# Kernel tuning notes

Hardware: AMD Instinct MI355X
Metric: run time of the kernel (lower is better)

Reference implementation:

```python
import jax, jax.numpy as jnp
import numpy as np

NUM_BASES = 8


def setup_inputs() -> dict:
    key = jax.random.key(0)
    ks = jax.random.split(key, 8)
    N, E = 100000, 1600000
    IN_F, OUT_F, NUM_RELS = 128, 128, 16
    si = IN_F // NUM_BASES   # 16
    so = OUT_F // NUM_BASES  # 16
    return {
        "h": jax.random.normal(ks[0], (N, IN_F), dtype=jnp.float32),
        "norm": jax.random.uniform(ks[1], (N, 1), dtype=jnp.float32),
        "edge_src": jax.random.randint(ks[2], (E,), 0, N, dtype=jnp.int32),
        "edge_dst": jax.random.randint(ks[3], (E,), 0, N, dtype=jnp.int32),
        "edge_type": jax.random.randint(ks[4], (E,), 0, NUM_RELS, dtype=jnp.int32),
        "weight": jax.random.normal(ks[5], (NUM_RELS, NUM_BASES * si * so), dtype=jnp.float32) * 0.1,
        "bias_param": jax.random.normal(ks[6], (OUT_F,), dtype=jnp.float32) * 0.1,
        "loop_weight": jax.random.normal(ks[7], (IN_F, OUT_F), dtype=jnp.float32) * 0.1,
    }


def reference(h, norm, edge_src, edge_dst, edge_type, weight, bias_param, loop_weight):
    N, in_feat = h.shape
    out_feat = loop_weight.shape[1]
    si = in_feat // NUM_BASES
    so = out_feat // NUM_BASES
    E = edge_type.shape[0]

    # self-loop message (dropout=0.0 -> identity)
    loop_message = h @ loop_weight                      # [N, out_feat]

    # msg_func: gather per-edge relation weight blocks and do block-diag bmm
    W = weight[edge_type].reshape(E, NUM_BASES, si, so)  # [E, B, si, so]
    src = h[edge_src].reshape(E, NUM_BASES, si)          # [E, B, si]
    msg = jnp.einsum("ebi,ebio->ebo", src, W).reshape(E, out_feat)

    # scatter-sum messages to destination nodes, rescale by norm
    agg = jax.ops.segment_sum(msg, edge_dst, num_segments=N)  # [N, out_feat]
    node_repr = agg * norm

    # bias + self-loop + activation
    node_repr = node_repr + bias_param + loop_message
    return jax.nn.relu(node_repr)
```

## Files before the change

kernel.cpp:

```cpp
#include <hip/hip_runtime.h>


__device__ __forceinline__ unsigned int f2bf(float f) {
  const unsigned int u = __float_as_uint(f);
  return (u + 0x7FFFu + ((u >> 16) & 1u)) >> 16;
}

__global__ __launch_bounds__(256) void rgcn_init_kernel(
    const float* __restrict__ h, const float* __restrict__ loop_w,
    const float* __restrict__ bias, float* __restrict__ out, int N) {
  __shared__ float lw[128 * 128];
  for (int idx = threadIdx.x; idx < 128 * 128 / 4; idx += 256) {
    ((float4*)lw)[idx] = ((const float4*)loop_w)[idx];
  }
  __syncthreads();

  const int lane = threadIdx.x & 63;
  const int wid = threadIdx.x >> 6;
  const int group0 = blockIdx.x * 4 + wid;
  const int ngroups = gridDim.x * 4;
  const int totgroups = (N + 3) >> 2;
  const float b0 = bias[lane];
  const float b1 = bias[64 + lane];

  for (int g = group0; g < totgroups; g += ngroups) {
    const int n0 = g * 4;
    const int nn = (N - n0 < 4) ? (N - n0) : 4;
    if (nn == 4) {
      const float* __restrict__ r0 = h + (size_t)n0 * 128;
      const float* __restrict__ r1 = r0 + 128;
      const float* __restrict__ r2 = r1 + 128;
      const float* __restrict__ r3 = r2 + 128;
      float a00 = b0, a01 = b1, a10 = b0, a11 = b1;
      float a20 = b0, a21 = b1, a30 = b0, a31 = b1;
#pragma unroll 4
      for (int k = 0; k < 128; ++k) {
        const float w0 = lw[k * 128 + lane];
        const float w1 = lw[k * 128 + 64 + lane];
        a00 = fmaf(r0[k], w0, a00); a01 = fmaf(r0[k], w1, a01);
        a10 = fmaf(r1[k], w0, a10); a11 = fmaf(r1[k], w1, a11);
        a20 = fmaf(r2[k], w0, a20); a21 = fmaf(r2[k], w1, a21);
        a30 = fmaf(r3[k], w0, a30); a31 = fmaf(r3[k], w1, a31);
      }
      float* __restrict__ o0 = out + (size_t)n0 * 128;
      o0[lane] = a00;        o0[64 + lane] = a01;
      o0[128 + lane] = a10;  o0[192 + lane] = a11;
      o0[256 + lane] = a20;  o0[320 + lane] = a21;
      o0[384 + lane] = a30;  o0[448 + lane] = a31;
    } else {
      for (int r = 0; r < nn; ++r) {
        const int n = n0 + r;
        const float* __restrict__ hr = h + (size_t)n * 128;
        float a0 = b0, a1 = b1;
#pragma unroll 4
        for (int k = 0; k < 128; ++k) {
          const float a = hr[k];
          a0 = fmaf(a, lw[k * 128 + lane], a0);
          a1 = fmaf(a, lw[k * 128 + 64 + lane], a1);
        }
        out[(size_t)n * 128 + lane] = a0;
        out[(size_t)n * 128 + 64 + lane] = a1;
      }
    }
  }
}

__global__ __launch_bounds__(1024) void rgcn_precompute_kernel(
    const float* __restrict__ h, const float* __restrict__ weight,
    unsigned int* __restrict__ M, int base, int cend) {
  const int lane = threadIdx.x & 63;
  const int t = threadIdx.x >> 6;
  const int b = lane >> 4;
  const int o = lane & 15;

  const float* __restrict__ wb = weight + t * 2048 + b * 256 + o;
  float wlo[16], whi[16];
#pragma unroll
  for (int i = 0; i < 16; ++i) {
    wlo[i] = wb[i * 16];
    whi[i] = wb[1024 + i * 16];
  }

  const int span = cend - base;
  const int n0 = base + (int)(((long)blockIdx.x * span) / gridDim.x);
  const int n1 = base + (int)(((long)(blockIdx.x + 1) * span) / gridDim.x);

#pragma unroll 2
  for (int n = n0; n < n1; ++n) {
    const float4* __restrict__ hp =
        (const float4*)(h + (size_t)n * 128) + (b << 2);
    const float4 x0 = hp[0], x1 = hp[1], x2 = hp[2], x3 = hp[3];
    const float4 y0 = hp[16], y1 = hp[17], y2 = hp[18], y3 = hp[19];

    float a0 = x0.x * wlo[0], a1 = x0.y * wlo[1];
    a0 = fmaf(x0.z, wlo[2], a0);  a1 = fmaf(x0.w, wlo[3], a1);
    a0 = fmaf(x1.x, wlo[4], a0);  a1 = fmaf(x1.y, wlo[5], a1);
    a0 = fmaf(x1.z, wlo[6], a0);  a1 = fmaf(x1.w, wlo[7], a1);
    a0 = fmaf(x2.x, wlo[8], a0);  a1 = fmaf(x2.y, wlo[9], a1);
    a0 = fmaf(x2.z, wlo[10], a0); a1 = fmaf(x2.w, wlo[11], a1);
    a0 = fmaf(x3.x, wlo[12], a0); a1 = fmaf(x3.y, wlo[13], a1);
    a0 = fmaf(x3.z, wlo[14], a0); a1 = fmaf(x3.w, wlo[15], a1);

    float c0 = y0.x * whi[0], c1 = y0.y * whi[1];
    c0 = fmaf(y0.z, whi[2], c0);  c1 = fmaf(y0.w, whi[3], c1);
    c0 = fmaf(y1.x, whi[4], c0);  c1 = fmaf(y1.y, whi[5], c1);
    c0 = fmaf(y1.z, whi[6], c0);  c1 = fmaf(y1.w, whi[7], c1);
    c0 = fmaf(y2.x, whi[8], c0);  c1 = fmaf(y2.y, whi[9], c1);
    c0 = fmaf(y2.z, whi[10], c0); c1 = fmaf(y2.w, whi[11], c1);
    c0 = fmaf(y3.x, whi[12], c0); c1 = fmaf(y3.y, whi[13], c1);
    c0 = fmaf(y3.z, whi[14], c0); c1 = fmaf(y3.w, whi[15], c1);

    const unsigned int pk = f2bf(a0 + a1) | (f2bf(c0 + c1) << 16);
    M[(((size_t)(n - base) << 4) | t) * 64 + lane] = pk;
  }
}

__global__ __launch_bounds__(256) void rgcn_zero_kernel(int* __restrict__ p,
                                                        int n) {
  for (int i = blockIdx.x * 256 + threadIdx.x; i < n; i += gridDim.x * 256)
    p[i] = 0;
}

__global__ __launch_bounds__(256) void rgcn_hist_kernel(
    const int* __restrict__ esrc, const int* __restrict__ edst,
    int* __restrict__ cnt, int E, int N, unsigned S) {
  for (int e = blockIdx.x * 256 + threadIdx.x; e < E; e += gridDim.x * 256) {
    const unsigned q = (unsigned)esrc[e] / S;
    atomicAdd(&cnt[(int)(q * (unsigned)N) + edst[e]], 1);
  }
}

__global__ __launch_bounds__(1024) void rgcn_scan_pass1(
    const int* __restrict__ cnt, int* __restrict__ partial, int bins) {
  __shared__ int sums[1024];
  const int t = threadIdx.x;
  const int base = blockIdx.x * 4096 + t * 4;
  int s = 0;
  if (base + 3 < bins) {
    const int4 v = *(const int4*)(cnt + base);
    s = v.x + v.y + v.z + v.w;
  } else {
    for (int j = 0; j < 4; ++j)
      if (base + j < bins) s += cnt[base + j];
  }
  sums[t] = s;
  __syncthreads();
  for (int off = 512; off > 0; off >>= 1) {
    if (t < off) sums[t] += sums[t + off];
    __syncthreads();
  }
  if (t == 0) partial[blockIdx.x] = sums[0];
}

__global__ __launch_bounds__(1024) void rgcn_scan_pass2(
    int* __restrict__ partial, int nb) {
  __shared__ int sc[1024];
  const int t = threadIdx.x;
  int v[4];
  int s = 0;
#pragma unroll
  for (int j = 0; j < 4; ++j) {
    const int i = t * 4 + j;
    v[j] = (i < nb) ? partial[i] : 0;
    s += v[j];
  }
  sc[t] = s;
  __syncthreads();
#pragma unroll
  for (int off = 1; off < 1024; off <<= 1) {
    const int add = (t >= off) ? sc[t - off] : 0;
    __syncthreads();
    sc[t] += add;
    __syncthreads();
  }
  int run = (t == 0) ? 0 : sc[t - 1];
#pragma unroll
  for (int j = 0; j < 4; ++j) {
    const int i = t * 4 + j;
    if (i < nb) partial[i] = run;
    run += v[j];
  }
}

__global__ __launch_bounds__(1024) void rgcn_scan_pass3(
    const int* __restrict__ cnt, const int* __restrict__ partial,
    int* __restrict__ row_ptr, int* __restrict__ cursor, int bins) {
  __shared__ int sums[1024];
  const int t = threadIdx.x;
  const int base = blockIdx.x * 4096 + t * 4;
  int v0 = 0, v1 = 0, v2 = 0, v3 = 0;
  if (base + 3 < bins) {
    const int4 v = *(const int4*)(cnt + base);
    v0 = v.x; v1 = v.y; v2 = v.z; v3 = v.w;
  } else {
    if (base < bins) v0 = cnt[base];
    if (base + 1 < bins) v1 = cnt[base + 1];
    if (base + 2 < bins) v2 = cnt[base + 2];
  }
  sums[t] = v0 + v1 + v2 + v3;
  __syncthreads();
#pragma unroll
  for (int off = 1; off < 1024; off <<= 1) {
    const int add = (t >= off) ? sums[t - off] : 0;
    __syncthreads();
    sums[t] += add;
    __syncthreads();
  }
  const int run = partial[blockIdx.x] + ((t == 0) ? 0 : sums[t - 1]);
  const int p0 = run, p1 = p0 + v0, p2 = p1 + v1, p3 = p2 + v2;
  if (base + 3 < bins) {
    *(int4*)(row_ptr + base) = make_int4(p0, p1, p2, p3);
    *(int4*)(cursor + base) = make_int4(p0, p1, p2, p3);
  } else {
    if (base < bins) { row_ptr[base] = p0; cursor[base] = p0; }
    if (base + 1 < bins) { row_ptr[base + 1] = p1; cursor[base + 1] = p1; }
    if (base + 2 < bins) { row_ptr[base + 2] = p2; cursor[base + 2] = p2; }
  }
}

__global__ void rgcn_set_kernel(int* __restrict__ p, int v) {
  if (threadIdx.x == 0) *p = v;
}

__global__ __launch_bounds__(256) void rgcn_scatter_kernel(
    const int* __restrict__ esrc, const int* __restrict__ edst,
    const int* __restrict__ etype, int* __restrict__ cursor,
    int* __restrict__ srec, int E, int N, unsigned S) {
  for (int e = blockIdx.x * 256 + threadIdx.x; e < E; e += gridDim.x * 256) {
    const unsigned s = (unsigned)esrc[e];
    const unsigned q = s / S;
    const int key = (int)(q * (unsigned)N) + edst[e];
    const int p = atomicAdd(&cursor[key], 1);
    srec[p] = (int)((s - q * S) << 4) | etype[e];
  }
}

__global__ __launch_bounds__(256) void rgcn_gather3_kernel(
    const float* __restrict__ norm, const int* __restrict__ srec,
    const int* __restrict__ rpc, const unsigned int* __restrict__ M,
    float* __restrict__ out, int N, int final_pass) {
  const int lane = threadIdx.x & 63;
  const int w0 = blockIdx.x * 4 + (threadIdx.x >> 6);
  const int nw = gridDim.x * 4;

  for (int d = w0; d < N; d += nw) {
    const int e0 = rpc[d];
    const int e1 = rpc[d + 1];
    if (!final_pass && e0 == e1) continue;

    float acc0 = 0.f, acc1 = 0.f;
    int e = e0;
    for (; e + 4 <= e1; e += 4) {
      const int r0 = srec[e], r1 = srec[e + 1], r2 = srec[e + 2],
                r3 = srec[e + 3];
      const unsigned int v0 = M[(size_t)r0 * 64 + lane];
      const unsigned int v1 = M[(size_t)r1 * 64 + lane];
      const unsigned int v2 = M[(size_t)r2 * 64 + lane];
      const unsigned int v3 = M[(size_t)r3 * 64 + lane];
      acc0 += __uint_as_float(v0 << 16);
      acc1 += __uint_as_float(v0 & 0xFFFF0000u);
      acc0 += __uint_as_float(v1 << 16);
      acc1 += __uint_as_float(v1 & 0xFFFF0000u);
      acc0 += __uint_as_float(v2 << 16);
      acc1 += __uint_as_float(v2 & 0xFFFF0000u);
      acc0 += __uint_as_float(v3 << 16);
      acc1 += __uint_as_float(v3 & 0xFFFF0000u);
    }
    for (; e < e1; ++e) {
      const unsigned int v = M[(size_t)srec[e] * 64 + lane];
      acc0 += __uint_as_float(v << 16);
      acc1 += __uint_as_float(v & 0xFFFF0000u);
    }

    const float nm = norm[d];
    float* __restrict__ op = out + ((size_t)d << 7);
    float o0 = fmaf(acc0, nm, op[lane]);
    float o1 = fmaf(acc1, nm, op[64 + lane]);
    if (final_pass) {
      o0 = fmaxf(o0, 0.f);
      o1 = fmaxf(o1, 0.f);
    }
    op[lane] = o0;
    op[64 + lane] = o1;
  }
}

__global__ __launch_bounds__(256) void rgcn_edge_kernel(
    const float* __restrict__ h, const float* __restrict__ norm,
    const int* __restrict__ esrc, const int* __restrict__ edst,
    const int* __restrict__ etype, const float* __restrict__ weight,
    float* __restrict__ out, int E) {
  const int lane = threadIdx.x & 63;
  const int wid = threadIdx.x >> 6;
  const int wave0 = blockIdx.x * 4 + wid;
  const int nwaves = gridDim.x * 4;
  const int b = lane >> 4;
  const int o = lane & 15;

  for (int e = wave0; e < E; e += nwaves) {
    const int src = esrc[e];
    const int dst = edst[e];
    const int et = etype[e];
    const float s_lo = h[src * 128 + lane];
    const float s_hi = h[src * 128 + 64 + lane];
    const float nrm = norm[dst];
    const float* __restrict__ Wb = weight + et * 2048 + b * 256 + o;
    float m0 = 0.f, m1 = 0.f;
#pragma unroll
    for (int i = 0; i < 16; ++i) {
      const float a_lo = __shfl(s_lo, (lane & 48) + i, 64);
      const float a_hi = __shfl(s_hi, (lane & 48) + i, 64);
      m0 = fmaf(a_lo, Wb[i * 16], m0);
      m1 = fmaf(a_hi, Wb[1024 + i * 16], m1);
    }
    atomicAdd(&out[dst * 128 + lane], m0 * nrm);
    atomicAdd(&out[dst * 128 + 64 + lane], m1 * nrm);
  }
}

__global__ __launch_bounds__(256) void rgcn_relu_kernel(float* __restrict__ out,
                                                        int total4) {
  int i = blockIdx.x * 256 + threadIdx.x;
  const int stride = gridDim.x * 256;
  for (; i < total4; i += stride) {
    float4 v = ((float4*)out)[i];
    v.x = fmaxf(v.x, 0.f);
    v.y = fmaxf(v.y, 0.f);
    v.z = fmaxf(v.z, 0.f);
    v.w = fmaxf(v.w, 0.f);
    ((float4*)out)[i] = v;
  }
}

extern "C" void kernel_launch(void* const* d_in, const int* in_sizes, int n_in,
                              void* d_out, int out_size, void* d_ws, size_t ws_size,
                              hipStream_t stream) {
  const float* h      = (const float*)d_in[0];
  const float* norm   = (const float*)d_in[1];
  const int*   esrc   = (const int*)d_in[2];
  const int*   edst   = (const int*)d_in[3];
  const int*   etype  = (const int*)d_in[4];
  const float* weight = (const float*)d_in[5];
  const float* bias   = (const float*)d_in[6];
  const float* loop_w = (const float*)d_in[7];
  float* out = (float*)d_out;

  const int N = in_sizes[0] / 128;
  const int E = in_sizes[2];
  const int nrels = in_sizes[5] / 2048;

  rgcn_init_kernel<<<2048, 256, 0, stream>>>(h, loop_w, bias, out, N);

  int C = -1, S = 0;
  size_t ofs_rp = 0, ofs_cur = 0, ofs_part = 0, ofs_srec = 0, ofs_M = 0;
  if (nrels == 16 && N >= 1 && N < (1 << 26)) {
    for (int cc = 1; cc <= 64; ++cc) {
      const size_t bins = (size_t)cc * (size_t)N;
      if (bins > (size_t)4096 * 4096) break;
      const int ss = (N + cc - 1) / cc;
      const size_t o_rp = (bins + 3) & ~(size_t)3;
      const size_t o_cur = (o_rp + bins + 1 + 3) & ~(size_t)3;
      const size_t o_part = (o_cur + bins + 3) & ~(size_t)3;
      const size_t o_srec = o_part + 4096;
      const size_t o_M = (o_srec + (size_t)E + 15) & ~(size_t)15;
      const size_t need = (o_M + (size_t)ss * 16 * 64) * 4;
      if (need <= ws_size) {
        C = cc; S = ss;
        ofs_rp = o_rp; ofs_cur = o_cur; ofs_part = o_part;
        ofs_srec = o_srec; ofs_M = o_M;
        break;
      }
    }
  }

  if (C >= 1) {
    const int bins = C * N;
    const int nb = (bins + 4095) / 4096;
    int* base    = (int*)d_ws;
    int* cnt     = base;
    int* row_ptr = base + ofs_rp;
    int* cursor  = base + ofs_cur;
    int* partial = base + ofs_part;
    int* srec    = base + ofs_srec;
    unsigned int* M = (unsigned int*)(base + ofs_M);

    rgcn_zero_kernel<<<1024, 256, 0, stream>>>(cnt, bins);
    rgcn_hist_kernel<<<2048, 256, 0, stream>>>(esrc, edst, cnt, E, N,
                                               (unsigned)S);
    rgcn_scan_pass1<<<nb, 1024, 0, stream>>>(cnt, partial, bins);
    rgcn_scan_pass2<<<1, 1024, 0, stream>>>(partial, nb);
    rgcn_scan_pass3<<<nb, 1024, 0, stream>>>(cnt, partial, row_ptr, cursor,
                                             bins);
    rgcn_set_kernel<<<1, 64, 0, stream>>>(row_ptr + bins, E);
    rgcn_scatter_kernel<<<2048, 256, 0, stream>>>(esrc, edst, etype, cursor,
                                                  srec, E, N, (unsigned)S);
    for (int c = 0; c < C; ++c) {
      const int cbase = c * S;
      const int cend = (cbase + S < N) ? (cbase + S) : N;
      if (cbase >= N) break;
      rgcn_precompute_kernel<<<256, 1024, 0, stream>>>(h, weight, M, cbase,
                                                       cend);
      rgcn_gather3_kernel<<<2048, 256, 0, stream>>>(
          norm, srec, row_ptr + (size_t)c * N, M, out, N,
          (c == C - 1) ? 1 : 0);
    }
  } else {
    rgcn_edge_kernel<<<4096, 256, 0, stream>>>(h, norm, esrc, edst, etype,
                                               weight, out, E);
    rgcn_relu_kernel<<<2048, 256, 0, stream>>>(out, (N * 128) / 4);
  }
}
```

Measured before the change: 899.5 us.

## Replace precomputed per-relation node table with dst-block/type sorted LDS aggregation

Drops the precompute of a bf16 per-node-per-relation message table and its chunked gather passes. Edges are now bucketed by (destination block of 16, relation type). One workgroup per destination block holds relation weights in registers, computes each edge message from gathered h rows via wave shuffles, and accumulates into LDS with atomics before a fused norm/add/relu epilogue. This removes the large M write/read traffic and the bf16 rounding, but adds per-edge FMA work, LDS atomic contention, and serialized per-type loops that may load-balance poorly.

Measured after the change: 1.887 ms. +109.8%, slower.

```diff
diff --git a/kernel.cpp b/kernel.cpp
--- a/kernel.cpp
+++ b/kernel.cpp
@@ -1,10 +1,5 @@
 #include <hip/hip_runtime.h>
 
-
-__device__ __forceinline__ unsigned int f2bf(float f) {
-  const unsigned int u = __float_as_uint(f);
-  return (u + 0x7FFFu + ((u >> 16) & 1u)) >> 16;
-}
 
 __global__ __launch_bounds__(256) void rgcn_init_kernel(
     const float* __restrict__ h, const float* __restrict__ loop_w,
@@ -65,68 +60,18 @@
   }
 }
 
-__global__ __launch_bounds__(1024) void rgcn_precompute_kernel(
-    const float* __restrict__ h, const float* __restrict__ weight,
-    unsigned int* __restrict__ M, int base, int cend) {
-  const int lane = threadIdx.x & 63;
-  const int t = threadIdx.x >> 6;
-  const int b = lane >> 4;
-  const int o = lane & 15;
-
-  const float* __restrict__ wb = weight + t * 2048 + b * 256 + o;
-  float wlo[16], whi[16];
-#pragma unroll
-  for (int i = 0; i < 16; ++i) {
-    wlo[i] = wb[i * 16];
-    whi[i] = wb[1024 + i * 16];
-  }
-
-  const int span = cend - base;
-  const int n0 = base + (int)(((long)blockIdx.x * span) / gridDim.x);
-  const int n1 = base + (int)(((long)(blockIdx.x + 1) * span) / gridDim.x);
-
-#pragma unroll 2
-  for (int n = n0; n < n1; ++n) {
-    const float4* __restrict__ hp =
-        (const float4*)(h + (size_t)n * 128) + (b << 2);
-    const float4 x0 = hp[0], x1 = hp[1], x2 = hp[2], x3 = hp[3];
-    const float4 y0 = hp[16], y1 = hp[17], y2 = hp[18], y3 = hp[19];
-
-    float a0 = x0.x * wlo[0], a1 = x0.y * wlo[1];
-    a0 = fmaf(x0.z, wlo[2], a0);  a1 = fmaf(x0.w, wlo[3], a1);
-    a0 = fmaf(x1.x, wlo[4], a0);  a1 = fmaf(x1.y, wlo[5], a1);
-    a0 = fmaf(x1.z, wlo[6], a0);  a1 = fmaf(x1.w, wlo[7], a1);
-    a0 = fmaf(x2.x, wlo[8], a0);  a1 = fmaf(x2.y, wlo[9], a1);
-    a0 = fmaf(x2.z, wlo[10], a0); a1 = fmaf(x2.w, wlo[11], a1);
-    a0 = fmaf(x3.x, wlo[12], a0); a1 = fmaf(x3.y, wlo[13], a1);
-    a0 = fmaf(x3.z, wlo[14], a0); a1 = fmaf(x3.w, wlo[15], a1);
-
-    float c0 = y0.x * whi[0], c1 = y0.y * whi[1];
-    c0 = fmaf(y0.z, whi[2], c0);  c1 = fmaf(y0.w, whi[3], c1);
-    c0 = fmaf(y1.x, whi[4], c0);  c1 = fmaf(y1.y, whi[5], c1);
-    c0 = fmaf(y1.z, whi[6], c0);  c1 = fmaf(y1.w, whi[7], c1);
-    c0 = fmaf(y2.x, whi[8], c0);  c1 = fmaf(y2.y, whi[9], c1);
-    c0 = fmaf(y2.z, whi[10], c0); c1 = fmaf(y2.w, whi[11], c1);
-    c0 = fmaf(y3.x, whi[12], c0); c1 = fmaf(y3.y, whi[13], c1);
-    c0 = fmaf(y3.z, whi[14], c0); c1 = fmaf(y3.w, whi[15], c1);
-
-    const unsigned int pk = f2bf(a0 + a1) | (f2bf(c0 + c1) << 16);
-    M[(((size_t)(n - base) << 4) | t) * 64 + lane] = pk;
-  }
-}
-
 __global__ __launch_bounds__(256) void rgcn_zero_kernel(int* __restrict__ p,
                                                         int n) {
   for (int i = blockIdx.x * 256 + threadIdx.x; i < n; i += gridDim.x * 256)
     p[i] = 0;
 }
 
-__global__ __launch_bounds__(256) void rgcn_hist_kernel(
-    const int* __restrict__ esrc, const int* __restrict__ edst,
-    int* __restrict__ cnt, int E, int N, unsigned S) {
+__global__ __launch_bounds__(256) void rgcn_hist2_kernel(
+    const int* __restrict__ edst, const int* __restrict__ etype,
+    int* __restrict__ cnt, int E) {
   for (int e = blockIdx.x * 256 + threadIdx.x; e < E; e += gridDim.x * 256) {
-    const unsigned q = (unsigned)esrc[e] / S;
-    atomicAdd(&cnt[(int)(q * (unsigned)N) + edst[e]], 1);
+    const int key = (edst[e] & ~15) | etype[e];
+    atomicAdd(&cnt[key], 1);
   }
 }
 
@@ -222,66 +167,87 @@
   if (threadIdx.x == 0) *p = v;
 }
 
-__global__ __launch_bounds__(256) void rgcn_scatter_kernel(
+__global__ __launch_bounds__(256) void rgcn_scatter2_kernel(
     const int* __restrict__ esrc, const int* __restrict__ edst,
     const int* __restrict__ etype, int* __restrict__ cursor,
-    int* __restrict__ srec, int E, int N, unsigned S) {
+    int* __restrict__ srec, int E) {
   for (int e = blockIdx.x * 256 + threadIdx.x; e < E; e += gridDim.x * 256) {
-    const unsigned s = (unsigned)esrc[e];
-    const unsigned q = s / S;
-    const int key = (int)(q * (unsigned)N) + edst[e];
+    const int d = edst[e];
+    const int key = (d & ~15) | etype[e];
     const int p = atomicAdd(&cursor[key], 1);
-    srec[p] = (int)((s - q * S) << 4) | etype[e];
-  }
-}
-
-__global__ __launch_bounds__(256) void rgcn_gather3_kernel(
-    const float* __restrict__ norm, const int* __restrict__ srec,
-    const int* __restrict__ rpc, const unsigned int* __restrict__ M,
-    float* __restrict__ out, int N, int final_pass) {
-  const int lane = threadIdx.x & 63;
-  const int w0 = blockIdx.x * 4 + (threadIdx.x >> 6);
-  const int nw = gridDim.x * 4;
-
-  for (int d = w0; d < N; d += nw) {
-    const int e0 = rpc[d];
-    const int e1 = rpc[d + 1];
-    if (!final_pass && e0 == e1) continue;
-
-    float acc0 = 0.f, acc1 = 0.f;
-    int e = e0;
-    for (; e + 4 <= e1; e += 4) {
-      const int r0 = srec[e], r1 = srec[e + 1], r2 = srec[e + 2],
-                r3 = srec[e + 3];
-      const unsigned int v0 = M[(size_t)r0 * 64 + lane];
-      const unsigned int v1 = M[(size_t)r1 * 64 + lane];
-      const unsigned int v2 = M[(size_t)r2 * 64 + lane];
-      const unsigned int v3 = M[(size_t)r3 * 64 + lane];
-      acc0 += __uint_as_float(v0 << 16);
-      acc1 += __uint_as_float(v0 & 0xFFFF0000u);
-      acc0 += __uint_as_float(v1 << 16);
-      acc1 += __uint_as_float(v1 & 0xFFFF0000u);
-      acc0 += __uint_as_float(v2 << 16);
-      acc1 += __uint_as_float(v2 & 0xFFFF0000u);
-      acc0 += __uint_as_float(v3 << 16);
-      acc1 += __uint_as_float(v3 & 0xFFFF0000u);
-    }
-    for (; e < e1; ++e) {
-      const unsigned int v = M[(size_t)srec[e] * 64 + lane];
-      acc0 += __uint_as_float(v << 16);
-      acc1 += __uint_as_float(v & 0xFFFF0000u);
-    }
-
-    const float nm = norm[d];
-    float* __restrict__ op = out + ((size_t)d << 7);
-    float o0 = fmaf(acc0, nm, op[lane]);
-    float o1 = fmaf(acc1, nm, op[64 + lane]);
-    if (final_pass) {
-      o0 = fmaxf(o0, 0.f);
-      o1 = fmaxf(o1, 0.f);
-    }
-    op[lane] = o0;
-    op[64 + lane] = o1;
+    srec[p] = (esrc[e] << 4) | (d & 15);
+  }
+}
+
+__global__ __launch_bounds__(256) void rgcn_edge_lds2_kernel(
+    const float* __restrict__ h, const float* __restrict__ norm,
+    const int* __restrict__ srec, const int* __restrict__ row_ptr,
+    const float* __restrict__ weight, float* __restrict__ out, int N) {
+  __shared__ float acc[16 * 128];
+  const int tid = threadIdx.x;
+  const int lane = tid & 63;
+  const int w = tid >> 6;
+  const int b = lane >> 4;
+  const int o = lane & 15;
+  const int r = blockIdx.x;
+
+  for (int i = tid; i < 16 * 128 / 4; i += 256)
+    ((float4*)acc)[i] = make_float4(0.f, 0.f, 0.f, 0.f);
+  __syncthreads();
+
+  for (int tt = 0; tt < 4; ++tt) {
+    const int t = w * 4 + tt;
+    const int e0 = row_ptr[r * 16 + t];
+    const int e1 = row_ptr[r * 16 + t + 1];
+    if (e0 == e1) continue;
+
+    const float* __restrict__ wb = weight + t * 2048 + b * 256 + o;
+    float wlo[16], whi[16];
+#pragma unroll
+    for (int i = 0; i < 16; ++i) {
+      wlo[i] = wb[i * 16];
+      whi[i] = wb[1024 + i * 16];
+    }
+
+    int recA = srec[e0];
+    float loA = h[(size_t)(recA >> 4) * 128 + lane];
+    float hiA = h[(size_t)(recA >> 4) * 128 + 64 + lane];
+
+    for (int e = e0; e < e1; ++e) {
+      const int rec = recA;
+      const float lo = loA, hi = hiA;
+      if (e + 1 < e1) {
+        recA = srec[e + 1];
+        loA = h[(size_t)(recA >> 4) * 128 + lane];
+        hiA = h[(size_t)(recA >> 4) * 128 + 64 + lane];
+      }
+      float m0 = 0.f, m1 = 0.f;
+#pragma unroll
+      for (int i = 0; i < 16; ++i) {
+        m0 = fmaf(__shfl(lo, (lane & 48) + i, 64), wlo[i], m0);
+        m1 = fmaf(__shfl(hi, (lane & 48) + i, 64), whi[i], m1);
+      }
+      const int dl = rec & 15;
+      atomicAdd(&acc[dl * 128 + lane], m0);
+      atomicAdd(&acc[dl * 128 + 64 + lane], m1);
+    }
+  }
+  __syncthreads();
+
+  for (int idx = tid; idx < 16 * 32; idx += 256) {
+    const int dl = idx >> 5;
+    const int c4 = idx & 31;
+    const int d = r * 16 + dl;
+    if (d < N) {
+      const float nm = norm[d];
+      const float4 a = ((const float4*)acc)[idx];
+      float4 ov = ((float4*)out)[(size_t)d * 32 + c4];
+      ov.x = fmaxf(fmaf(a.x, nm, ov.x), 0.f);
+      ov.y = fmaxf(fmaf(a.y, nm, ov.y), 0.f);
+      ov.z = fmaxf(fmaf(a.z, nm, ov.z), 0.f);
+      ov.w = fmaxf(fmaf(a.w, nm, ov.w), 0.f);
+      ((float4*)out)[(size_t)d * 32 + c4] = ov;
+    }
   }
 }
 
@@ -351,59 +317,35 @@
 
   rgcn_init_kernel<<<2048, 256, 0, stream>>>(h, loop_w, bias, out, N);
 
-  int C = -1, S = 0;
-  size_t ofs_rp = 0, ofs_cur = 0, ofs_part = 0, ofs_srec = 0, ofs_M = 0;
-  if (nrels == 16 && N >= 1 && N < (1 << 26)) {
-    for (int cc = 1; cc <= 64; ++cc) {
-      const size_t bins = (size_t)cc * (size_t)N;
-      if (bins > (size_t)4096 * 4096) break;
-      const int ss = (N + cc - 1) / cc;
-      const size_t o_rp = (bins + 3) & ~(size_t)3;
-      const size_t o_cur = (o_rp + bins + 1 + 3) & ~(size_t)3;
-      const size_t o_part = (o_cur + bins + 3) & ~(size_t)3;
-      const size_t o_srec = o_part + 4096;
-      const size_t o_M = (o_srec + (size_t)E + 15) & ~(size_t)15;
-      const size_t need = (o_M + (size_t)ss * 16 * 64) * 4;
-      if (need <= ws_size) {
-        C = cc; S = ss;
-        ofs_rp = o_rp; ofs_cur = o_cur; ofs_part = o_part;
-        ofs_srec = o_srec; ofs_M = o_M;
-        break;
-      }
-    }
-  }
-
-  if (C >= 1) {
-    const int bins = C * N;
-    const int nb = (bins + 4095) / 4096;
+  const int nR = (N + 15) >> 4;
+  const int bins = nR * 16;
+  const size_t o_rp = ((size_t)bins + 3) & ~(size_t)3;
+  const size_t o_cur = (o_rp + bins + 1 + 3) & ~(size_t)3;
+  const size_t o_part = (o_cur + bins + 3) & ~(size_t)3;
+  const size_t o_srec = o_part + 4096;
+  const size_t need = (o_srec + (size_t)E) * 4;
+  const int nb = (bins + 4095) / 4096;
+
+  if (nrels == 16 && N >= 1 && N < (1 << 26) && nb <= 4096 &&
+      ws_size >= need) {
     int* base    = (int*)d_ws;
     int* cnt     = base;
-    int* row_ptr = base + ofs_rp;
-    int* cursor  = base + ofs_cur;
-    int* partial = base + ofs_part;
-    int* srec    = base + ofs_srec;
-    unsigned int* M = (unsigned int*)(base + ofs_M);
-
-    rgcn_zero_kernel<<<1024, 256, 0, stream>>>(cnt, bins);
-    rgcn_hist_kernel<<<2048, 256, 0, stream>>>(esrc, edst, cnt, E, N,
-                                               (unsigned)S);
+    int* row_ptr = base + o_rp;
+    int* cursor  = base + o_cur;
+    int* partial = base + o_part;
+    int* srec    = base + o_srec;
+
+    rgcn_zero_kernel<<<256, 256, 0, stream>>>(cnt, bins);
+    rgcn_hist2_kernel<<<2048, 256, 0, stream>>>(edst, etype, cnt, E);
     rgcn_scan_pass1<<<nb, 1024, 0, stream>>>(cnt, partial, bins);
     rgcn_scan_pass2<<<1, 1024, 0, stream>>>(partial, nb);
     rgcn_scan_pass3<<<nb, 1024, 0, stream>>>(cnt, partial, row_ptr, cursor,
                                              bins);
     rgcn_set_kernel<<<1, 64, 0, stream>>>(row_ptr + bins, E);
-    rgcn_scatter_kernel<<<2048, 256, 0, stream>>>(esrc, edst, etype, cursor,
-                                                  srec, E, N, (unsigned)S);
-    for (int c = 0; c < C; ++c) {
-      const int cbase = c * S;
-      const int cend = (cbase + S < N) ? (cbase + S) : N;
-      if (cbase >= N) break;
-      rgcn_precompute_kernel<<<256, 1024, 0, stream>>>(h, weight, M, cbase,
-                                                       cend);
-      rgcn_gather3_kernel<<<2048, 256, 0, stream>>>(
-          norm, srec, row_ptr + (size_t)c * N, M, out, N,
-          (c == C - 1) ? 1 : 0);
-    }
+    rgcn_scatter2_kernel<<<2048, 256, 0, stream>>>(esrc, edst, etype, cursor,
+                                                   srec, E);
+    rgcn_edge_lds2_kernel<<<nR, 256, 0, stream>>>(h, norm, srec, row_ptr,
+                                                  weight, out, N);
   } else {
     rgcn_edge_kernel<<<4096, 256, 0, stream>>>(h, norm, esrc, edst, etype,
                                                weight, out, E);
```
